# Performance work log

Hardware: AMD Instinct MI355X
Metric: run time of the kernel (lower is better)

## Reference

```python
import jax, jax.numpy as jnp
import numpy as np

C = 8      # num_categories
T = 1000   # num_steps
N = 16     # batch of graphs
n = 256    # nodes per graph


def _schedule(num_categories, num_steps):
    """Exactly replicates CategoricalDiffusion.__init__ buffers (fp64 -> fp32)."""
    qT = np.ones(num_categories) / num_categories
    steps = np.arange(num_steps + 1, dtype=np.float64) / num_steps
    alphas_bar = np.cos((steps + 0.008) / 1.008 * np.pi / 2)
    betas = np.minimum(1 - alphas_bar[1:] / alphas_bar[:-1], 0.999)
    eye = np.eye(num_categories)
    Qs = (1 - betas)[:, None, None] * eye + betas[:, None, None] * qT[None, :, None]
    Qbs = alphas_bar[:, None, None] * eye + (1 - alphas_bar)[:, None, None] * qT[None, :, None]
    return Qs.astype(np.float32), Qbs.astype(np.float32)


def setup_inputs() -> dict:
    key = jax.random.key(0)
    k1, k2, k3 = jax.random.split(key, 3)
    Qs_np, Qbs_np = _schedule(C, T)
    x_t = jax.random.randint(k1, (N, n, n), 0, C)                      # current noisy categories
    pred = jax.random.normal(k2, (N, n, n, C), dtype=jnp.float32)      # model logits over x_0
    t = jax.random.randint(k3, (N,), 1, T)                             # timestep per sample (>=1 so Qbs[t-1] is valid)
    return {"x_t": x_t, "pred": pred, "t": t,
            "Qs": jnp.asarray(Qs_np), "Qbs": jnp.asarray(Qbs_np)}


def reference(x_t, pred, t, Qs, Qbs):
    """q_reverse_sample: sample x_{t-1} ~ sum_x q(x_{t-1} | x, x_t) q(x | x_t)."""
    # left_term = Qs[t, :, x_t] -> (N, n, n, C) ; last axis indexes x_{t-1}
    left = Qs[t[:, None, None], :, x_t]
    # right_term = Qbs[t-1] -> (N, C, C) ; axes (x, x_{t-1})
    right = Qbs[t - 1]
    # posterior over x_{t-1} for every hypothesized x_0: (N, n, n, C_x, C_xtm1)
    posterior = left[:, :, :, None, :] * right[:, None, None, :, :]
    posterior = posterior / posterior.sum(-1, keepdims=True)
    x_probs = jax.nn.softmax(pred, axis=-1)                            # (N, n, n, C)
    # marginalize over x_0: (N, n, n, C)
    ancestral_probs = jnp.einsum('bijxc,bijx->bijc', posterior, x_probs)
    # categorical sample via Gumbel-max (equivalent to th.multinomial)
    g = jax.random.gumbel(jax.random.key(42), ancestral_probs.shape, dtype=ancestral_probs.dtype)
    x_t_1 = jnp.argmax(jnp.log(ancestral_probs) + g, axis=-1)
    x_0 = jnp.argmax(x_probs, axis=-1)
    nonzero = (t > 0)[:, None, None]
    out = jnp.where(nonzero, x_t_1, x_0)
    return out, ancestral_probs
```

## Files before the change

### kernel.cpp

```cpp
#include <hip/hip_runtime.h>
#include <stdint.h>

#pragma clang fp contract(off)

#define NPIX (16 * 256 * 256)
#define NCAT 8

__device__ __forceinline__ uint32_t rotl32(uint32_t x, int r) {
  return (x << r) | (x >> (32 - r));
}

__device__ __forceinline__ uint32_t tf_bits(uint32_t idx) {
  const uint32_t ks0 = 0u;
  const uint32_t ks1 = 42u;
  const uint32_t ks2 = 0x1BD11BDAu ^ ks0 ^ ks1;
  uint32_t x0 = 0u + ks0;
  uint32_t x1 = idx + ks1;
#define TF4(ra, rb, rc, rd)                  \
  x0 += x1; x1 = rotl32(x1, ra); x1 ^= x0;   \
  x0 += x1; x1 = rotl32(x1, rb); x1 ^= x0;   \
  x0 += x1; x1 = rotl32(x1, rc); x1 ^= x0;   \
  x0 += x1; x1 = rotl32(x1, rd); x1 ^= x0;
  TF4(13, 15, 26, 6)  x0 += ks1; x1 += ks2 + 1u;
  TF4(17, 29, 16, 24) x0 += ks2; x1 += ks0 + 2u;
  TF4(13, 15, 26, 6)  x0 += ks0; x1 += ks1 + 3u;
  TF4(17, 29, 16, 24) x0 += ks1; x1 += ks2 + 4u;
  TF4(13, 15, 26, 6)  x0 += ks2; x1 += ks0 + 5u;
#undef TF4
  return x0 ^ x1;
}

__device__ __forceinline__ float gumbel_at(uint32_t idx) {
  const float kTiny = 1.1754943508222875e-38f;
  uint32_t bits = tf_bits(idx);
  float f = __uint_as_float((bits >> 9) | 0x3f800000u) - 1.0f;
  f = __fadd_rn(__fmul_rn(f, 1.0f), kTiny);
  f = fmaxf(kTiny, f);
  return -logf(-logf(f));
}

__global__ __launch_bounds__(256) void catdiff_sample_kernel(
    const int* __restrict__ x_t, const float* __restrict__ pred,
    const int* __restrict__ t, const float* __restrict__ Qs,
    const float* __restrict__ Qbs, float* __restrict__ out_idx,
    float* __restrict__ out_probs) {
  __shared__ float sL[64];
  __shared__ float sR[64];

  const int p = blockIdx.x * 256 + threadIdx.x;
  const int b = p >> 16;
  const int tb = t[b];

  if (threadIdx.x < 64) {
    sL[threadIdx.x] = Qs[tb * 64 + threadIdx.x];
  } else if (threadIdx.x < 128) {
    sR[threadIdx.x - 64] = Qbs[(tb - 1) * 64 + (threadIdx.x - 64)];
  }
  __syncthreads();

  const int xt = x_t[p];

  float left[NCAT];
#pragma unroll
  for (int c = 0; c < NCAT; ++c) left[c] = sL[c * 8 + xt];

  const float4 pr0 = *reinterpret_cast<const float4*>(pred + (size_t)p * 8);
  const float4 pr1 = *reinterpret_cast<const float4*>(pred + (size_t)p * 8 + 4);
  float lg[NCAT] = {pr0.x, pr0.y, pr0.z, pr0.w, pr1.x, pr1.y, pr1.z, pr1.w};
  float m = lg[0];
#pragma unroll
  for (int c = 1; c < NCAT; ++c) m = fmaxf(m, lg[c]);
  float e[NCAT];
#pragma unroll
  for (int c = 0; c < NCAT; ++c) e[c] = expf(lg[c] - m);
  float s = 0.0f;
#pragma unroll
  for (int c = 0; c < NCAT; ++c) s = __fadd_rn(s, e[c]);
  float xp[NCAT];
#pragma unroll
  for (int c = 0; c < NCAT; ++c) xp[c] = e[c] / s;

  float anc[NCAT];
#pragma unroll
  for (int c = 0; c < NCAT; ++c) anc[c] = 0.0f;
#pragma unroll
  for (int X = 0; X < NCAT; ++X) {
    float denom = 0.0f;
#pragma unroll
    for (int c = 0; c < NCAT; ++c)
      denom = __fadd_rn(denom, __fmul_rn(left[c], sR[X * 8 + c]));
#pragma unroll
    for (int c = 0; c < NCAT; ++c) {
      float post = __fmul_rn(left[c], sR[X * 8 + c]) / denom;
      anc[c] = __fadd_rn(anc[c], __fmul_rn(post, xp[X]));
    }
  }

  const uint32_t gbase = (uint32_t)p * 8u;
  float bestv = __fadd_rn(logf(anc[0]), gumbel_at(gbase + 0u));
  int besti = 0;
#pragma unroll
  for (int c = 1; c < NCAT; ++c) {
    float v = __fadd_rn(logf(anc[c]), gumbel_at(gbase + (uint32_t)c));
    if (v > bestv) { bestv = v; besti = c; }
  }

  out_idx[p] = (float)besti;
  float4 o0 = make_float4(anc[0], anc[1], anc[2], anc[3]);
  float4 o1 = make_float4(anc[4], anc[5], anc[6], anc[7]);
  *reinterpret_cast<float4*>(out_probs + (size_t)p * 8) = o0;
  *reinterpret_cast<float4*>(out_probs + (size_t)p * 8 + 4) = o1;
}

extern "C" void kernel_launch(void* const* d_in, const int* in_sizes, int n_in,
                              void* d_out, int out_size, void* d_ws,
                              size_t ws_size, hipStream_t stream) {
  (void)in_sizes; (void)n_in; (void)out_size; (void)d_ws; (void)ws_size;
  const int*   x_t  = (const int*)d_in[0];
  const float* pred = (const float*)d_in[1];
  const int*   t    = (const int*)d_in[2];
  const float* Qs   = (const float*)d_in[3];
  const float* Qbs  = (const float*)d_in[4];
  float* out0 = (float*)d_out;
  float* out1 = out0 + NPIX;

  dim3 grid(NPIX / 256), block(256);
  hipLaunchKernelGGL(catdiff_sample_kernel, grid, block, 0, stream,
                     x_t, pred, t, Qs, Qbs, out0, out1);
}
```

Before: 137.9 us.

## Precompute per-block posterior table in shared memory instead of per-pixel divides

Each block now computes the 8x8 denominators and the full 8x8x8 normalized posterior table once in shared memory, so each pixel reads one row indexed by its x_t instead of doing 64 divides and redundant products. The pred and x_t global loads are moved before the barriers to overlap their latency with table setup. In exchange it adds two extra __syncthreads and about 8KB of shared memory per block, and the per-pixel row reads depend on x_t, which may cause LDS bank conflicts.

```diff
diff --git a/kernel.cpp b/kernel.cpp
--- a/kernel.cpp
+++ b/kernel.cpp
@@ -5,6 +5,7 @@
 
 #define NPIX (16 * 256 * 256)
 #define NCAT 8
+#define MSTRIDE 260
 
 __device__ __forceinline__ uint32_t rotl32(uint32_t x, int r) {
   return (x << r) | (x >> (32 - r));
@@ -46,26 +47,47 @@
     float* __restrict__ out_probs) {
   __shared__ float sL[64];
   __shared__ float sR[64];
+  __shared__ float sDen[64];
+  __shared__ float sM[8 * MSTRIDE];
 
-  const int p = blockIdx.x * 256 + threadIdx.x;
-  const int b = p >> 16;
+  const int tid = threadIdx.x;
+  const int p = blockIdx.x * 256 + tid;
+  const int b = blockIdx.x >> 8;
+
+  const float4 pr0 = *reinterpret_cast<const float4*>(pred + (size_t)p * 8);
+  const float4 pr1 = *reinterpret_cast<const float4*>(pred + (size_t)p * 8 + 4);
+  const int xt = x_t[p];
   const int tb = t[b];
 
-  if (threadIdx.x < 64) {
-    sL[threadIdx.x] = Qs[tb * 64 + threadIdx.x];
-  } else if (threadIdx.x < 128) {
-    sR[threadIdx.x - 64] = Qbs[(tb - 1) * 64 + (threadIdx.x - 64)];
+  if (tid < 64) {
+    sL[tid] = Qs[tb * 64 + tid];
+  } else if (tid < 128) {
+    sR[tid - 64] = Qbs[(tb - 1) * 64 + (tid - 64)];
   }
   __syncthreads();
 
-  const int xt = x_t[p];
+  if (tid < 64) {
+    const int x = tid >> 3;
+    const int X = tid & 7;
+    float d = 0.0f;
+#pragma unroll
+    for (int c = 0; c < NCAT; ++c)
+      d = __fadd_rn(d, __fmul_rn(sL[c * 8 + x], sR[X * 8 + c]));
+    sDen[tid] = d;
+  }
+  __syncthreads();
 
-  float left[NCAT];
+  {
 #pragma unroll
-  for (int c = 0; c < NCAT; ++c) left[c] = sL[c * 8 + xt];
+    for (int k = 0; k < 2; ++k) {
+      const int e = tid * 2 + k;
+      const int x = e >> 6, X = (e >> 3) & 7, c = e & 7;
+      sM[x * MSTRIDE + X * 8 + c] =
+          __fmul_rn(sL[c * 8 + x], sR[X * 8 + c]) / sDen[(x << 3) | X];
+    }
+  }
+  __syncthreads();
 
-  const float4 pr0 = *reinterpret_cast<const float4*>(pred + (size_t)p * 8);
-  const float4 pr1 = *reinterpret_cast<const float4*>(pred + (size_t)p * 8 + 4);
   float lg[NCAT] = {pr0.x, pr0.y, pr0.z, pr0.w, pr1.x, pr1.y, pr1.z, pr1.w};
   float m = lg[0];
 #pragma unroll
@@ -83,17 +105,19 @@
   float anc[NCAT];
 #pragma unroll
   for (int c = 0; c < NCAT; ++c) anc[c] = 0.0f;
+  const float* Mrow = &sM[xt * MSTRIDE];
 #pragma unroll
   for (int X = 0; X < NCAT; ++X) {
-    float denom = 0.0f;
-#pragma unroll
-    for (int c = 0; c < NCAT; ++c)
-      denom = __fadd_rn(denom, __fmul_rn(left[c], sR[X * 8 + c]));
-#pragma unroll
-    for (int c = 0; c < NCAT; ++c) {
-      float post = __fmul_rn(left[c], sR[X * 8 + c]) / denom;
-      anc[c] = __fadd_rn(anc[c], __fmul_rn(post, xp[X]));
-    }
+    const float4 m0 = *reinterpret_cast<const float4*>(Mrow + X * 8);
+    const float4 m1 = *reinterpret_cast<const float4*>(Mrow + X * 8 + 4);
+    anc[0] = __fadd_rn(anc[0], __fmul_rn(m0.x, xp[X]));
+    anc[1] = __fadd_rn(anc[1], __fmul_rn(m0.y, xp[X]));
+    anc[2] = __fadd_rn(anc[2], __fmul_rn(m0.z, xp[X]));
+    anc[3] = __fadd_rn(anc[3], __fmul_rn(m0.w, xp[X]));
+    anc[4] = __fadd_rn(anc[4], __fmul_rn(m1.x, xp[X]));
+    anc[5] = __fadd_rn(anc[5], __fmul_rn(m1.y, xp[X]));
+    anc[6] = __fadd_rn(anc[6], __fmul_rn(m1.z, xp[X]));
+    anc[7] = __fadd_rn(anc[7], __fmul_rn(m1.w, xp[X]));
   }
 
   const uint32_t gbase = (uint32_t)p * 8u;
```

After: 117.4 us. -14.9%, faster.
